# Performance work log

Hardware: AMD Instinct MI355X
Metric: run time of the kernel (lower is better)

## Reference

```python
import jax, jax.numpy as jnp
import numpy as np

B, S, E, H = 2, 2048, 1024, 16
D = E // H
SCALE = D ** -0.5


def setup_inputs() -> dict:
    key = jax.random.key(0)
    k1, k2, k3, k4, k5 = jax.random.split(key, 5)
    x = jax.random.normal(k1, (B, S, E), dtype=jnp.float32)
    # torch Linear weights: [out, in]
    W_attn = jax.random.normal(k2, (3 * E, E), dtype=jnp.float32) * (E ** -0.5)
    b_attn = jax.random.normal(k3, (3 * E,), dtype=jnp.float32) * 0.02
    W_proj = jax.random.normal(k4, (E, E), dtype=jnp.float32) * (E ** -0.5)
    b_proj = jax.random.normal(k5, (E,), dtype=jnp.float32) * 0.02
    mask = jnp.tril(jnp.ones((S, S), dtype=jnp.int32))[None, None]  # causal [1,1,S,S]
    return {"x": x, "W_attn": W_attn, "b_attn": b_attn,
            "W_proj": W_proj, "b_proj": b_proj, "mask": mask}


def reference(x, W_attn, b_attn, W_proj, b_proj, mask):
    # fused qkv projection: [B,S,3E]
    qkv = jnp.einsum('bse,fe->bsf', x, W_attn) + b_attn
    q, k, v = jnp.split(qkv, 3, axis=-1)
    # split heads -> [B,H,S,D]
    def heads(t):
        return t.reshape(B, S, H, D).transpose(0, 2, 1, 3)
    q, k, v = heads(q), heads(k), heads(v)
    # scaled dot-product attention with causal mask
    w = jnp.einsum('bhqd,bhkd->bhqk', q, k) * SCALE
    w = jnp.where(mask == 0, jnp.finfo(w.dtype).min, w)
    w = jax.nn.softmax(w, axis=-1)  # attn dropout p=0 (eval)
    o = jnp.einsum('bhqk,bhkd->bhqd', w, v)
    # merge heads -> [B,S,E]
    o = o.transpose(0, 2, 1, 3).reshape(B, S, E)
    out = jnp.einsum('bse,fe->bsf', o, W_proj) + b_proj  # resid dropout p=0
    return out
```

## Files before the change

kernel.cpp:

```cpp
#include <hip/hip_runtime.h>
#include <hip/hip_bf16.h>

typedef unsigned short u16;
typedef unsigned int u32;
typedef float f32x4 __attribute__((ext_vector_type(4)));
typedef short bf16x8 __attribute__((ext_vector_type(8)));

#define BB 2
#define SS 2048
#define EE 1024
#define HH 16
#define DD 64
#define QSCALE 0.18033688011f

__device__ __forceinline__ u16 f2bf(float f) {
    union { u32 i; float f; } x; x.f = f;
    return (u16)((x.i + 0x7FFFu + ((x.i >> 16) & 1u)) >> 16);
}
__device__ __forceinline__ u32 pkbf(float a, float b) {
    __hip_bfloat162 h = __float22bfloat162_rn(make_float2(a, b));
    union { __hip_bfloat162 h; u32 u; } c; c.h = h; return c.u;
}

#define MFMA16(a, b, c) __builtin_amdgcn_mfma_f32_16x16x32_bf16((a), (b), (c), 0, 0, 0)

__device__ __forceinline__ void gld16(const u16* g, u16* l) {
    __builtin_amdgcn_global_load_lds(
        (const __attribute__((address_space(1))) void*)g,
        (__attribute__((address_space(3))) void*)l,
        16, 0, 0);
}

__global__ __launch_bounds__(256) void convert_all(
    const float* __restrict__ x, const float* __restrict__ wa,
    const float* __restrict__ wp, u16* __restrict__ dst)
{
    const size_t n0 = (size_t)4096 * 1024;
    const size_t n1 = n0 + (size_t)3072 * 1024;
    size_t i = ((size_t)blockIdx.x * 256 + threadIdx.x) * 4;
    const float* s;
    size_t off;
    if (i < n0)      { s = x;  off = 0;  }
    else if (i < n1) { s = wa; off = n0; }
    else             { s = wp; off = n1; }
    float4 v = *(const float4*)(s + (i - off));
    uint2 o;
    o.x = pkbf(v.x, v.y);
    o.y = pkbf(v.z, v.w);
    *(uint2*)(dst + i) = o;
}

__global__ __launch_bounds__(512, 4) void gemm_qkv(
    const u16* __restrict__ A, const u16* __restrict__ B, const float* __restrict__ bias,
    u16* __restrict__ Qo, u16* __restrict__ Ko, u16* __restrict__ Vto)
{
    __shared__ __align__(16) u16 SMEM[2][16384];
    const int n0 = blockIdx.x * 128, m0 = blockIdx.y * 128;
    const int tid = threadIdx.x;
    const int wave = tid >> 6, lane = tid & 63;
    const int l16 = lane & 15, quad = lane >> 4;
    const int wm = wave >> 2, wn = wave & 3;
    const int ldr = lane >> 3;
    const int csw = ((lane & 7) ^ ldr) * 8;

    f32x4 acc[4][2];
#pragma unroll
    for (int i = 0; i < 4; ++i)
#pragma unroll
        for (int j = 0; j < 2; ++j) acc[i][j] = f32x4{0.f, 0.f, 0.f, 0.f};

    const int aorb = wave >> 2;
    const u16* stgsrc = aorb ? B : A;
    const int stgbase = aorb ? n0 : m0;
    const int stgoff = aorb ? 8192 : 0;

    auto stage = [&](int k0, int buf) {
        u16* stgbuf = &SMEM[buf][stgoff];
#pragma unroll
        for (int t = 0; t < 4; ++t) {
            const int c = (wave & 3) * 4 + t;
            const int row = c * 8 + ldr;
            gld16(stgsrc + (size_t)(stgbase + row) * 1024 + k0 + csw,
                  &stgbuf[c * 512 + lane * 8]);
        }
    };

    stage(0, 0);
    for (int k0 = 0; k0 < 1024; k0 += 64) {
        const int cur = (k0 >> 6) & 1;
        __syncthreads();
        if (k0 + 64 < 1024) stage(k0 + 64, cur ^ 1);
        const u16* As = SMEM[cur];
        const u16* Bs = SMEM[cur] + 8192;
#pragma unroll
        for (int ks = 0; ks < 2; ++ks) {
            bf16x8 af[4], bf[2];
#pragma unroll
            for (int i = 0; i < 4; ++i)
                af[i] = *(const bf16x8*)&As[(wm * 64 + i * 16 + l16) * 64 +
                                            ((ks * 4 + quad) ^ (l16 & 7)) * 8];
#pragma unroll
            for (int j = 0; j < 2; ++j)
                bf[j] = *(const bf16x8*)&Bs[(wn * 32 + j * 16 + l16) * 64 +
                                            ((ks * 4 + quad) ^ (l16 & 7)) * 8];
#pragma unroll
            for (int i = 0; i < 4; ++i)
#pragma unroll
                for (int j = 0; j < 2; ++j)
                    acc[i][j] = MFMA16(af[i], bf[j], acc[i][j]);
        }
    }

    const int part = blockIdx.x >> 3;
    const int hbase = (blockIdx.x & 7) << 1;
    if (part != 2) {
        const int h = hbase + (wn >> 1);
#pragma unroll
        for (int j = 0; j < 2; ++j) {
            const int f = n0 + wn * 32 + j * 16 + l16;
            const int d = f & 63;
            const float bj = bias[f];
#pragma unroll
            for (int i = 0; i < 4; ++i) {
#pragma unroll
                for (int r = 0; r < 4; ++r) {
                    const int m = m0 + wm * 64 + i * 16 + quad * 4 + r;
                    const int b = m >> 11, s = m & 2047;
                    const float val = acc[i][j][r] + bj;
                    if (part == 0)
                        Qo[(((size_t)(b * HH + h)) * SS + s) * DD + d] = f2bf(val * QSCALE);
                    else
                        Ko[(((size_t)(b * HH + h)) * SS + s) * DD + d] = f2bf(val);
                }
            }
        }
    } else {
        u16* T = SMEM[0];
#pragma unroll
        for (int wmr = 0; wmr < 2; ++wmr) {
            __syncthreads();
            if (wm == wmr) {
#pragma unroll
                for (int j = 0; j < 2; ++j) {
                    const float bj = bias[n0 + wn * 32 + j * 16 + l16];
#pragma unroll
                    for (int i = 0; i < 4; ++i) {
                        uint2 pw;
                        pw.x = pkbf(acc[i][j][0] + bj, acc[i][j][1] + bj);
                        pw.y = pkbf(acc[i][j][2] + bj, acc[i][j][3] + bj);
                        *(uint2*)&T[(wn * 32 + j * 16 + l16) * 72 + i * 16 + quad * 4] = pw;
                    }
                }
            }
            __syncthreads();
            const int frow = tid >> 2;
            const int qtr = tid & 3;
            const int h = hbase + (frow >> 6);
            const int d = frow & 63;
            const int mg = m0 + wmr * 64;
            const int b = mg >> 11, sbase = mg & 2047;
            u16* dstrow = Vto + (((size_t)(b * HH + h)) * DD + d) * SS + sbase;
#pragma unroll
            for (int l = 0; l < 4; ++l) {
                const int mo = qtr * 16 + l * 4;
                *(uint2*)(dstrow + mo) = *(const uint2*)&T[frow * 72 + mo];
            }
        }
    }
}

__global__ __launch_bounds__(512, 4) void gemm_proj(
    const u16* __restrict__ A, const u16* __restrict__ B, const float* __restrict__ bias,
    float* __restrict__ out)
{
    __shared__ __align__(16) u16 SMEM[2][12288];
    const int n0 = blockIdx.x * 128, m0 = blockIdx.y * 64;
    const int tid = threadIdx.x;
    const int wave = tid >> 6, lane = tid & 63;
    const int l16 = lane & 15, quad = lane >> 4;
    const int wm = wave >> 2, wn = wave & 3;
    const int ldr = lane >> 3;
    const int csw = ((lane & 7) ^ ldr) * 8;

    f32x4 acc[2][2];
#pragma unroll
    for (int i = 0; i < 2; ++i)
#pragma unroll
        for (int j = 0; j < 2; ++j) acc[i][j] = f32x4{0.f, 0.f, 0.f, 0.f};

    auto stage = [&](int k0, int buf) {
#pragma unroll
        for (int t = 0; t < 3; ++t) {
            const int c = wave * 3 + t;
            if (c < 8) {
                const int row = c * 8 + ldr;
                gld16(A + (size_t)(m0 + row) * 1024 + k0 + csw,
                      &SMEM[buf][c * 512 + lane * 8]);
            } else {
                const int c2 = c - 8;
                const int row = c2 * 8 + ldr;
                gld16(B + (size_t)(n0 + row) * 1024 + k0 + csw,
                      &SMEM[buf][4096 + c2 * 512 + lane * 8]);
            }
        }
    };

    stage(0, 0);
    for (int k0 = 0; k0 < 1024; k0 += 64) {
        const int cur = (k0 >> 6) & 1;
        __syncthreads();
        if (k0 + 64 < 1024) stage(k0 + 64, cur ^ 1);
        const u16* As = SMEM[cur];
        const u16* Bs = SMEM[cur] + 4096;
#pragma unroll
        for (int ks = 0; ks < 2; ++ks) {
            bf16x8 af[2], bf[2];
#pragma unroll
            for (int i = 0; i < 2; ++i)
                af[i] = *(const bf16x8*)&As[(wm * 32 + i * 16 + l16) * 64 +
                                            ((ks * 4 + quad) ^ (l16 & 7)) * 8];
#pragma unroll
            for (int j = 0; j < 2; ++j)
                bf[j] = *(const bf16x8*)&Bs[(wn * 32 + j * 16 + l16) * 64 +
                                            ((ks * 4 + quad) ^ (l16 & 7)) * 8];
#pragma unroll
            for (int i = 0; i < 2; ++i)
#pragma unroll
                for (int j = 0; j < 2; ++j)
                    acc[i][j] = MFMA16(af[i], bf[j], acc[i][j]);
        }
    }
#pragma unroll
    for (int j = 0; j < 2; ++j) {
        const int f = n0 + wn * 32 + j * 16 + l16;
        const float bj = bias[f];
#pragma unroll
        for (int i = 0; i < 2; ++i) {
#pragma unroll
            for (int r = 0; r < 4; ++r) {
                const int m = m0 + wm * 32 + i * 16 + quad * 4 + r;
                out[(size_t)m * EE + f] = acc[i][j][r] + bj;
            }
        }
    }
}

__global__ __launch_bounds__(256, 2) void attn(
    const u16* __restrict__ Q, const u16* __restrict__ K, const u16* __restrict__ VT,
    u16* __restrict__ O)
{
    const int p = blockIdx.y;
    const int bh = blockIdx.x;
    const int tid = threadIdx.x;
    const int wave = tid >> 6, lane = tid & 63;
    const int l16 = lane & 15, quad = lane >> 4;
    const int ldr = lane >> 3;
    const int csw = ((lane & 7) ^ ldr) * 8;
    __shared__ __align__(16) u16 Ks[2][2][64 * 64];
    __shared__ __align__(16) u16 Vts[2][2][64 * 64];
    __shared__ __align__(16) u16 Ps[64 * 72];

    const u16* qptr = Q + (size_t)bh * SS * DD;
    const u16* kptr = K + (size_t)bh * SS * DD;
    const u16* vtptr = VT + (size_t)bh * DD * SS;
    const int b = bh >> 4, h = bh & 15;

    auto stage = [&](int t, int buf, int sub) {
#pragma unroll
        for (int c = 0; c < 2; ++c) {
            const int a0 = wave * 2 + c;
            const int row = a0 * 8 + ldr;
            gld16(kptr + (size_t)(t * 64 + row) * DD + csw,
                  &Ks[buf][sub][a0 * 512 + lane * 8]);
            gld16(vtptr + (size_t)row * SS + t * 64 + csw,
                  &Vts[buf][sub][a0 * 512 + lane * 8]);
        }
    };

    for (int half = 0; half < 2; ++half) {
        const int qb = half ? p : 31 - p;
        const int qrow = qb * 64 + wave * 16 + l16;
        bf16x8 bq[2];
#pragma unroll
        for (int ks = 0; ks < 2; ++ks)
            bq[ks] = *(const bf16x8*)(qptr + (size_t)qrow * DD + ks * 32 + quad * 8);

        float lp = 0.f;
        f32x4 o_acc[4];
#pragma unroll
        for (int j = 0; j < 4; ++j) o_acc[j] = f32x4{0.f, 0.f, 0.f, 0.f};

        auto tile_compute = [&](const u16* Kb, const u16* Vb, int t) {
            f32x4 s[4];
#pragma unroll
            for (int j = 0; j < 4; ++j) s[j] = f32x4{0.f, 0.f, 0.f, 0.f};
            __builtin_amdgcn_s_setprio(1);
#pragma unroll
            for (int ks = 0; ks < 2; ++ks) {
#pragma unroll
                for (int j = 0; j < 4; ++j) {
                    bf16x8 ak = *(const bf16x8*)&Kb[(j * 16 + l16) * 64 +
                                                    ((ks * 4 + quad) ^ (l16 & 7)) * 8];
                    s[j] = MFMA16(ak, bq[ks], s[j]);
                }
            }
            __builtin_amdgcn_s_setprio(0);
            if (t == qb) {
#pragma unroll
                for (int j = 0; j < 4; ++j)
#pragma unroll
                    for (int r = 0; r < 4; ++r) {
                        const int key = t * 64 + j * 16 + quad * 4 + r;
                        if (key > qrow) s[j][r] = -INFINITY;
                    }
            }
#pragma unroll
            for (int j = 0; j < 4; ++j) {
                const float p0 = __builtin_amdgcn_exp2f(s[j][0]);
                const float p1 = __builtin_amdgcn_exp2f(s[j][1]);
                const float p2 = __builtin_amdgcn_exp2f(s[j][2]);
                const float p3 = __builtin_amdgcn_exp2f(s[j][3]);
                lp += (p0 + p1) + (p2 + p3);
                uint2 pw; pw.x = pkbf(p0, p1); pw.y = pkbf(p2, p3);
                *(uint2*)&Ps[(wave * 16 + l16) * 72 + j * 16 + quad * 4] = pw;
            }
            __builtin_amdgcn_s_setprio(1);
#pragma unroll
            for (int ks = 0; ks < 2; ++ks) {
                bf16x8 bp = *(const bf16x8*)&Ps[(wave * 16 + l16) * 72 + ks * 32 + quad * 8];
#pragma unroll
                for (int j = 0; j < 4; ++j) {
                    bf16x8 av = *(const bf16x8*)&Vb[(j * 16 + l16) * 64 +
                                                    ((ks * 4 + quad) ^ (l16 & 7)) * 8];
                    o_acc[j] = MFMA16(av, bp, o_acc[j]);
                }
            }
            __builtin_amdgcn_s_setprio(0);
        };

        __syncthreads();
        stage(0, 0, 0);
        stage(qb < 1 ? qb : 1, 0, 1);

        for (int kb = 0; kb <= qb; kb += 2) {
            const int cur = (kb >> 1) & 1;
            __syncthreads();
            if (kb + 2 <= qb) {
                stage(kb + 2, cur ^ 1, 0);
                const int t3 = kb + 3 > qb ? qb : kb + 3;
                stage(t3, cur ^ 1, 1);
            }
            tile_compute(Ks[cur][0], Vts[cur][0], kb);
            if (kb + 1 <= qb)
                tile_compute(Ks[cur][1], Vts[cur][1], kb + 1);
        }

        float l = lp;
        l += __shfl_xor(l, 16);
        l += __shfl_xor(l, 32);
        const float inv = 1.0f / l;
#pragma unroll
        for (int j = 0; j < 4; ++j) {
            uint2 o4;
            o4.x = pkbf(o_acc[j][0] * inv, o_acc[j][1] * inv);
            o4.y = pkbf(o_acc[j][2] * inv, o_acc[j][3] * inv);
            *(uint2*)&O[((size_t)(b * SS + qrow)) * EE + h * DD + j * 16 + quad * 4] = o4;
        }
    }
}

extern "C" void kernel_launch(void* const* d_in, const int* in_sizes, int n_in,
                              void* d_out, int out_size, void* d_ws, size_t ws_size,
                              hipStream_t stream) {
    const float* x      = (const float*)d_in[0];
    const float* W_attn = (const float*)d_in[1];
    const float* b_attn = (const float*)d_in[2];
    const float* W_proj = (const float*)d_in[3];
    const float* b_proj = (const float*)d_in[4];
    float* out = (float*)d_out;

    u16* xb  = (u16*)d_ws;
    u16* wab = xb + (size_t)4096 * 1024;
    u16* wpb = wab + (size_t)3072 * 1024;
    u16* qw  = wpb + (size_t)1024 * 1024;
    u16* kw  = qw + (size_t)BB * HH * SS * DD;
    u16* vtw = kw + (size_t)BB * HH * SS * DD;
    u16* ow  = xb;

    convert_all<<<8192, 256, 0, stream>>>(x, W_attn, W_proj, xb);
    gemm_qkv<<<dim3(24, 32), 512, 0, stream>>>(xb, wab, b_attn, qw, kw, vtw);
    attn<<<dim3(32, 16), 256, 0, stream>>>(qw, kw, vtw, ow);
    gemm_proj<<<dim3(8, 64), 512, 0, stream>>>(ow, wpb, b_proj, out);
}
```

Before: 180.2 us.

## Share K/V tiles across two query tiles per attention block with 8 waves

Result: slower. 190.1 us (+5.5%).

```diff
diff --git a/kernel.cpp b/kernel.cpp
--- a/kernel.cpp
+++ b/kernel.cpp
@@ -245,41 +245,40 @@
     }
 }
 
-__global__ __launch_bounds__(256, 2) void attn(
+__global__ __launch_bounds__(512, 2) void attn(
     const u16* __restrict__ Q, const u16* __restrict__ K, const u16* __restrict__ VT,
     u16* __restrict__ O)
 {
-    const int p = blockIdx.y;
+    const int y = blockIdx.y;
     const int bh = blockIdx.x;
     const int tid = threadIdx.x;
     const int wave = tid >> 6, lane = tid & 63;
+    const int wq = wave >> 2;
+    const int wv = wave & 3;
     const int l16 = lane & 15, quad = lane >> 4;
     const int ldr = lane >> 3;
     const int csw = ((lane & 7) ^ ldr) * 8;
-    __shared__ __align__(16) u16 Ks[2][2][64 * 64];
-    __shared__ __align__(16) u16 Vts[2][2][64 * 64];
-    __shared__ __align__(16) u16 Ps[64 * 72];
+    __shared__ __align__(16) u16 Ks[2][64 * 64];
+    __shared__ __align__(16) u16 Vts[2][64 * 64];
+    __shared__ __align__(16) u16 Ps[128 * 72];
 
     const u16* qptr = Q + (size_t)bh * SS * DD;
     const u16* kptr = K + (size_t)bh * SS * DD;
     const u16* vtptr = VT + (size_t)bh * DD * SS;
     const int b = bh >> 4, h = bh & 15;
 
-    auto stage = [&](int t, int buf, int sub) {
-#pragma unroll
-        for (int c = 0; c < 2; ++c) {
-            const int a0 = wave * 2 + c;
-            const int row = a0 * 8 + ldr;
-            gld16(kptr + (size_t)(t * 64 + row) * DD + csw,
-                  &Ks[buf][sub][a0 * 512 + lane * 8]);
-            gld16(vtptr + (size_t)row * SS + t * 64 + csw,
-                  &Vts[buf][sub][a0 * 512 + lane * 8]);
-        }
+    auto stage = [&](int t, int buf) {
+        const int row = wave * 8 + ldr;
+        gld16(kptr + (size_t)(t * 64 + row) * DD + csw,
+              &Ks[buf][wave * 512 + lane * 8]);
+        gld16(vtptr + (size_t)row * SS + t * 64 + csw,
+              &Vts[buf][wave * 512 + lane * 8]);
     };
 
     for (int half = 0; half < 2; ++half) {
-        const int qb = half ? p : 31 - p;
-        const int qrow = qb * 64 + wave * 16 + l16;
+        const int t = half ? y : 15 - y;
+        const int qt = 2 * t + wq;
+        const int qrow = qt * 64 + wv * 16 + l16;
         bf16x8 bq[2];
 #pragma unroll
         for (int ks = 0; ks < 2; ++ks)
@@ -290,69 +289,64 @@
 #pragma unroll
         for (int j = 0; j < 4; ++j) o_acc[j] = f32x4{0.f, 0.f, 0.f, 0.f};
 
-        auto tile_compute = [&](const u16* Kb, const u16* Vb, int t) {
-            f32x4 s[4];
-#pragma unroll
-            for (int j = 0; j < 4; ++j) s[j] = f32x4{0.f, 0.f, 0.f, 0.f};
-            __builtin_amdgcn_s_setprio(1);
-#pragma unroll
-            for (int ks = 0; ks < 2; ++ks) {
+        const int kend = 2 * t + 1;
+
+        __syncthreads();
+        stage(0, 0);
+
+        for (int kb = 0; kb <= kend; ++kb) {
+            const int cur = kb & 1;
+            __syncthreads();
+            if (kb < kend) stage(kb + 1, cur ^ 1);
+
+            if (kb <= qt) {
+                f32x4 s[4];
+#pragma unroll
+                for (int j = 0; j < 4; ++j) s[j] = f32x4{0.f, 0.f, 0.f, 0.f};
+                __builtin_amdgcn_s_setprio(1);
+#pragma unroll
+                for (int ks = 0; ks < 2; ++ks) {
+#pragma unroll
+                    for (int j = 0; j < 4; ++j) {
+                        bf16x8 ak = *(const bf16x8*)&Ks[cur][(j * 16 + l16) * 64 +
+                                                        ((ks * 4 + quad) ^ (l16 & 7)) * 8];
+                        s[j] = MFMA16(ak, bq[ks], s[j]);
+                    }
+                }
+                __builtin_amdgcn_s_setprio(0);
+                if (kb == qt) {
+#pragma unroll
+                    for (int j = 0; j < 4; ++j)
+#pragma unroll
+                        for (int r = 0; r < 4; ++r) {
+                            const int key = kb * 64 + j * 16 + quad * 4 + r;
+                            if (key > qrow) s[j][r] = -INFINITY;
+                        }
+                }
 #pragma unroll
                 for (int j = 0; j < 4; ++j) {
-                    bf16x8 ak = *(const bf16x8*)&Kb[(j * 16 + l16) * 64 +
-                                                    ((ks * 4 + quad) ^ (l16 & 7)) * 8];
-                    s[j] = MFMA16(ak, bq[ks], s[j]);
-                }
-            }
-            __builtin_amdgcn_s_setprio(0);
-            if (t == qb) {
-#pragma unroll
-                for (int j = 0; j < 4; ++j)
-#pragma unroll
-                    for (int r = 0; r < 4; ++r) {
-                        const int key = t * 64 + j * 16 + quad * 4 + r;
-                        if (key > qrow) s[j][r] = -INFINITY;
+                    const float p0 = __builtin_amdgcn_exp2f(s[j][0]);
+                    const float p1 = __builtin_amdgcn_exp2f(s[j][1]);
+                    const float p2 = __builtin_amdgcn_exp2f(s[j][2]);
+                    const float p3 = __builtin_amdgcn_exp2f(s[j][3]);
+                    lp += (p0 + p1) + (p2 + p3);
+                    uint2 pw; pw.x = pkbf(p0, p1); pw.y = pkbf(p2, p3);
+                    *(uint2*)&Ps[(wave * 16 + l16) * 72 + j * 16 + quad * 4] = pw;
+                }
+                __builtin_amdgcn_s_setprio(1);
+#pragma unroll
+                for (int ks = 0; ks < 2; ++ks) {
+                    bf16x8 bp = *(const bf16x8*)&Ps[(wave * 16 + l16) * 72 +
+                                                    ks * 32 + quad * 8];
+#pragma unroll
+                    for (int j = 0; j < 4; ++j) {
+                        bf16x8 av = *(const bf16x8*)&Vts[cur][(j * 16 + l16) * 64 +
+                                                        ((ks * 4 + quad) ^ (l16 & 7)) * 8];
+                        o_acc[j] = MFMA16(av, bp, o_acc[j]);
                     }
-            }
-#pragma unroll
-            for (int j = 0; j < 4; ++j) {
-                const float p0 = __builtin_amdgcn_exp2f(s[j][0]);
-                const float p1 = __builtin_amdgcn_exp2f(s[j][1]);
-                const float p2 = __builtin_amdgcn_exp2f(s[j][2]);
-                const float p3 = __builtin_amdgcn_exp2f(s[j][3]);
-                lp += (p0 + p1) + (p2 + p3);
-                uint2 pw; pw.x = pkbf(p0, p1); pw.y = pkbf(p2, p3);
-                *(uint2*)&Ps[(wave * 16 + l16) * 72 + j * 16 + quad * 4] = pw;
-            }
-            __builtin_amdgcn_s_setprio(1);
-#pragma unroll
-            for (int ks = 0; ks < 2; ++ks) {
-                bf16x8 bp = *(const bf16x8*)&Ps[(wave * 16 + l16) * 72 + ks * 32 + quad * 8];
-#pragma unroll
-                for (int j = 0; j < 4; ++j) {
-                    bf16x8 av = *(const bf16x8*)&Vb[(j * 16 + l16) * 64 +
-                                                    ((ks * 4 + quad) ^ (l16 & 7)) * 8];
-                    o_acc[j] = MFMA16(av, bp, o_acc[j]);
-                }
-            }
-            __builtin_amdgcn_s_setprio(0);
-        };
-
-        __syncthreads();
-        stage(0, 0, 0);
-        stage(qb < 1 ? qb : 1, 0, 1);
-
-        for (int kb = 0; kb <= qb; kb += 2) {
-            const int cur = (kb >> 1) & 1;
-            __syncthreads();
-            if (kb + 2 <= qb) {
-                stage(kb + 2, cur ^ 1, 0);
-                const int t3 = kb + 3 > qb ? qb : kb + 3;
-                stage(t3, cur ^ 1, 1);
-            }
-            tile_compute(Ks[cur][0], Vts[cur][0], kb);
-            if (kb + 1 <= qb)
-                tile_compute(Ks[cur][1], Vts[cur][1], kb + 1);
+                }
+                __builtin_amdgcn_s_setprio(0);
+            }
         }
 
         float l = lp;
@@ -389,6 +383,6 @@
 
     convert_all<<<8192, 256, 0, stream>>>(x, W_attn, W_proj, xb);
     gemm_qkv<<<dim3(24, 32), 512, 0, stream>>>(xb, wab, b_attn, qw, kw, vtw);
-    attn<<<dim3(32, 16), 256, 0, stream>>>(qw, kw, vtw, ow);
+    attn<<<dim3(32, 8), 512, 0, stream>>>(qw, kw, vtw, ow);
     gemm_proj<<<dim3(8, 64), 512, 0, stream>>>(ow, wpb, b_proj, out);
 }
```
